# Performance work log

Measured on AMD Instinct MI355X. Metric: run time of the kernel, lower is better.

The kernel has to match this reference:

```python
import jax, jax.numpy as jnp
import numpy as np

B, T, D, H = 4, 2048, 1024, 16
HD = D // H  # head_dim = 64


def setup_inputs() -> dict:
    key = jax.random.key(0)
    ks = jax.random.split(key, 5)
    s = 0.02
    return {
        "x": jax.random.normal(ks[0], (B, T, D), dtype=jnp.float32),
        "Wq": jax.random.normal(ks[1], (D, D), dtype=jnp.float32) * s,
        "Wk": jax.random.normal(ks[2], (D, D), dtype=jnp.float32) * s,
        "Wv": jax.random.normal(ks[3], (D, D), dtype=jnp.float32) * s,
        "Wp": jax.random.normal(ks[4], (D, D), dtype=jnp.float32) * s,
    }


def reference(x, Wq, Wk, Wv, Wp):
    b, t, d = x.shape
    # QKV projections (bias=False), reshape to (b, h, t, hd)
    q = (x @ Wq.T).reshape(b, t, H, HD).transpose(0, 2, 1, 3)
    k = (x @ Wk.T).reshape(b, t, H, HD).transpose(0, 2, 1, 3)
    v = (x @ Wv.T).reshape(b, t, H, HD).transpose(0, 2, 1, 3)
    # scaled scores with causal mask
    scores = jnp.einsum("bhqd,bhkd->bhqk", q, k) / jnp.sqrt(jnp.float32(HD))
    causal = jnp.triu(jnp.ones((t, t), dtype=bool), k=1)
    scores = jnp.where(causal, -jnp.inf, scores)
    weights = jax.nn.softmax(scores, axis=-1)
    # dropout = 0.0 / eval mode -> identity
    ctx = jnp.einsum("bhqk,bhkd->bhqd", weights, v)
    ctx = ctx.transpose(0, 2, 1, 3).reshape(b, t, d)
    return ctx @ Wp.T
```

## Files before the change

### kernel.cpp

```cpp
#include <hip/hip_runtime.h>

typedef unsigned short u16;
typedef unsigned int u32;
typedef __attribute__((ext_vector_type(8))) short short8;
typedef __attribute__((ext_vector_type(4))) short short4_t;
typedef __attribute__((ext_vector_type(4))) float float4_t;

#define T_SEQ 2048
#define DMODEL 1024
#define NH 16
#define HD 64

#define GLL16(g, l) __builtin_amdgcn_global_load_lds( \
    (const __attribute__((address_space(1))) u32*)(g), \
    (__attribute__((address_space(3))) u32*)(l), 16, 0, 0)

__device__ inline u16 f2b(float f) {
  u32 x = __builtin_bit_cast(u32, f);
  x += 0x7fffu + ((x >> 16) & 1u);
  return (u16)(x >> 16);
}

__global__ __launch_bounds__(256) void conv_f2b(
    const float* __restrict__ x, const float* __restrict__ wq,
    const float* __restrict__ wk, const float* __restrict__ wv,
    const float* __restrict__ wp, u16* __restrict__ xb, u16* __restrict__ wb) {
  const size_t SZc = (size_t)8192 * 1024, WSZc = (size_t)1024 * 1024;
  size_t i = ((size_t)blockIdx.x * 256 + threadIdx.x) * 8;
  const float* s; u16* d; size_t off;
  if (i < SZc) { s = x; d = xb; off = i; }
  else {
    size_t j = i - SZc;
    size_t w = j >> 20;
    off = j & (WSZc - 1);
    s = (w == 0) ? wq : (w == 1) ? wk : (w == 2) ? wv : wp;
    d = wb + w * WSZc;
  }
  float4_t a = *(const float4_t*)(s + off);
  float4_t b = *(const float4_t*)(s + off + 4);
  short8 o;
  o[0] = (short)f2b(a[0]); o[1] = (short)f2b(a[1]);
  o[2] = (short)f2b(a[2]); o[3] = (short)f2b(a[3]);
  o[4] = (short)f2b(b[0]); o[5] = (short)f2b(b[1]);
  o[6] = (short)f2b(b[2]); o[7] = (short)f2b(b[3]);
  *(short8*)(d + off) = o;
}

__global__ __launch_bounds__(256) void gemm_bt(
    const u16* __restrict__ A,
    const u16* __restrict__ B0, const u16* __restrict__ B1, const u16* __restrict__ B2,
    u16* __restrict__ C0, u16* __restrict__ C1, u16* __restrict__ C2,
    float* __restrict__ Cf,
    int N, int Kd, int vtz, int of32, int scz, float cscale)
{
  const u16* Bp = (blockIdx.z == 0) ? B0 : ((blockIdx.z == 1) ? B1 : B2);
  u16* Cp = (blockIdx.z == 0) ? C0 : ((blockIdx.z == 1) ? C1 : C2);
  const bool vt = ((int)blockIdx.z == vtz);
  const float cs = ((int)blockIdx.z == scz) ? cscale : 1.0f;
  __shared__ u16 As[128 * 32];
  __shared__ u16 Bs[128 * 32];
  const int tid = threadIdx.x;
  const int lane = tid & 63;
  const int li = lane & 15;
  const int quad = lane >> 4;
  const int wv = tid >> 6;
  const int wm = (wv >> 1) * 64;
  const int wn = (wv & 1) * 64;
  const size_t bm = (size_t)blockIdx.x * 128;
  const size_t bn = (size_t)blockIdx.y * 128;

  float4_t acc[4][4];
  const float4_t z4 = {0.f, 0.f, 0.f, 0.f};
#pragma unroll
  for (int i = 0; i < 4; i++)
#pragma unroll
    for (int j = 0; j < 4; j++) acc[i][j] = z4;

  const int c0 = tid, c1 = tid + 256;
  const int r0 = c0 >> 2, e0 = (c0 & 3) * 8;
  const int r1 = c1 >> 2, e1 = (c1 & 3) * 8;

  for (int k0 = 0; k0 < Kd; k0 += 32) {
    __syncthreads();
    GLL16(A + (bm + r0) * Kd + k0 + e0, &As[c0 * 8]);
    GLL16(A + (bm + r1) * Kd + k0 + e1, &As[c1 * 8]);
    GLL16(Bp + (bn + r0) * Kd + k0 + e0, &Bs[c0 * 8]);
    GLL16(Bp + (bn + r1) * Kd + k0 + e1, &Bs[c1 * 8]);
    __syncthreads();
    short8 af[4], bf[4];
#pragma unroll
    for (int i = 0; i < 4; i++)
      af[i] = *(const short8*)&As[(wm + i * 16 + li) * 32 + quad * 8];
#pragma unroll
    for (int j = 0; j < 4; j++)
      bf[j] = *(const short8*)&Bs[(wn + j * 16 + li) * 32 + quad * 8];
#pragma unroll
    for (int i = 0; i < 4; i++)
#pragma unroll
      for (int j = 0; j < 4; j++)
        acc[i][j] = __builtin_amdgcn_mfma_f32_16x16x32_bf16(bf[j], af[i], acc[i][j], 0, 0, 0);
  }

  if (of32) {
#pragma unroll
    for (int i = 0; i < 4; i++)
#pragma unroll
      for (int j = 0; j < 4; j++) {
        size_t row = bm + wm + (size_t)(i * 16 + li);
        size_t col = bn + wn + (size_t)(j * 16 + quad * 4);
        *(float4_t*)&Cf[row * (size_t)N + col] = acc[i][j];
      }
  } else if (!vt) {
#pragma unroll
    for (int i = 0; i < 4; i++)
#pragma unroll
      for (int j = 0; j < 4; j++) {
        size_t row = bm + wm + (size_t)(i * 16 + li);
        size_t col = bn + wn + (size_t)(j * 16 + quad * 4);
        short4_t o;
#pragma unroll
        for (int r = 0; r < 4; r++) o[r] = (short)f2b(acc[i][j][r] * cs);
        *(short4_t*)&Cp[row * (size_t)N + col] = o;
      }
  } else {
#pragma unroll
    for (int i = 0; i < 4; i++) {
      size_t row = bm + wm + (size_t)(i * 16 + li);
      size_t bb = row >> 11;
      size_t tt = row & 2047;
#pragma unroll
      for (int j = 0; j < 4; j++) {
        size_t col = bn + wn + (size_t)(j * 16 + quad * 4);
#pragma unroll
        for (int r = 0; r < 4; r++)
          Cp[(bb * 1024 + col + r) * 2048 + tt] = f2b(acc[i][j][r]);
      }
    }
  }
}

#define LROW 72
__global__ __launch_bounds__(512) void attn_fwd(const u16* __restrict__ Qb,
                                                const u16* __restrict__ Kb,
                                                const u16* __restrict__ Vtb,
                                                u16* __restrict__ Ob) {
  __shared__ u16 Qs[128 * LROW];
  __shared__ u16 Kds[2][64 * LROW];
  __shared__ u16 Vds[2][64 * LROW];
  const int bh = blockIdx.y;
  const int bidx = bh >> 4;
  const int tid = threadIdx.x;
  const int lane = tid & 63;
  const int wv = tid >> 6;
  const int li = lane & 15;
  const int quad = lane >> 4;
  const size_t qkBase = ((size_t)bidx * T_SEQ) * DMODEL + (size_t)(bh & 15) * HD;
  const size_t vBase = (size_t)bh * HD * T_SEQ;
  const int krow = tid >> 3;
  const int kc8 = (tid & 7) * 8;
  const int kld = krow * LROW + kc8;
  const float4_t z4 = {0.f, 0.f, 0.f, 0.f};

#pragma unroll 1
  for (int ph = 0; ph < 2; ph++) {
    const int qblk = ph ? (int)blockIdx.x : (15 - (int)blockIdx.x);
    const int q0 = qblk * 128;
    const int ktmax = 2 * qblk + 1;
    const int qg0 = q0 + wv * 16;

    __syncthreads();
#pragma unroll
    for (int t = 0; t < 4; t++) {
      int slot = tid + t * 512;
      int row = slot >> 4, hc = slot & 15;
      *(short4_t*)&Qs[row * LROW + hc * 4] =
          *(const short4_t*)&Qb[qkBase + (size_t)(q0 + row) * DMODEL + hc * 4];
    }
    short8 kpre = *(const short8*)&Kb[qkBase + (size_t)krow * DMODEL + kc8];
    short8 vpre = *(const short8*)&Vtb[vBase + (size_t)krow * T_SEQ + kc8];
    __syncthreads();
    short8 qf[2];
    {
      const int row = wv * 16 + li;
#pragma unroll
      for (int s = 0; s < 2; s++)
        qf[s] = *(const short8*)&Qs[row * LROW + s * 32 + quad * 8];
    }
    *(short8*)&Kds[0][kld] = kpre;
    *(short8*)&Vds[0][kld] = vpre;
    kpre = *(const short8*)&Kb[qkBase + (size_t)(64 + krow) * DMODEL + kc8];
    vpre = *(const short8*)&Vtb[vBase + (size_t)krow * T_SEQ + 64 + kc8];

    float4_t accO[4];
#pragma unroll
    for (int dt = 0; dt < 4; dt++) accO[dt] = z4;
    float l_i = 0.f;

    for (int kt = 0; kt <= ktmax; kt++) {
      const int k0 = kt * 64;
      const int cb = kt & 1;
      __syncthreads();
      if (kt < ktmax) {
        *(short8*)&Kds[cb ^ 1][kld] = kpre;
        *(short8*)&Vds[cb ^ 1][kld] = vpre;
        if (kt + 1 < ktmax) {
          const int kn = k0 + 128;
          kpre = *(const short8*)&Kb[qkBase + (size_t)(kn + krow) * DMODEL + kc8];
          vpre = *(const short8*)&Vtb[vBase + (size_t)krow * T_SEQ + kn + kc8];
        }
      }
      if (k0 > qg0 + 15) continue;

      float4_t st[4];
#pragma unroll
      for (int jt = 0; jt < 4; jt++) {
        float4_t c4 = z4;
        const int row = jt * 16 + li;
#pragma unroll
        for (int s = 0; s < 2; s++) {
          short8 kf = *(const short8*)&Kds[cb][row * LROW + s * 32 + quad * 8];
          c4 = __builtin_amdgcn_mfma_f32_16x16x32_bf16(kf, qf[s], c4, 0, 0, 0);
        }
        st[jt] = c4;
      }

      short4_t pf[4];
      if (k0 + 63 > qg0) {
        const int ig = qg0 + li;
#pragma unroll
        for (int jt = 0; jt < 4; jt++)
#pragma unroll
          for (int r = 0; r < 4; r++) {
            int jg = k0 + jt * 16 + quad * 4 + r;
            float p = (jg <= ig) ? __builtin_amdgcn_exp2f(st[jt][r]) : 0.f;
            l_i += p;
            pf[jt][r] = (short)(__builtin_bit_cast(u32, p) >> 16);
          }
      } else {
#pragma unroll
        for (int jt = 0; jt < 4; jt++)
#pragma unroll
          for (int r = 0; r < 4; r++) {
            float p = __builtin_amdgcn_exp2f(st[jt][r]);
            l_i += p;
            pf[jt][r] = (short)(__builtin_bit_cast(u32, p) >> 16);
          }
      }

#pragma unroll
      for (int dt = 0; dt < 4; dt++) {
        const int d = dt * 16 + li;
#pragma unroll
        for (int jt = 0; jt < 4; jt++) {
          short4_t vf = *(const short4_t*)&Vds[cb][d * LROW + jt * 16 + quad * 4];
          accO[dt] = __builtin_amdgcn_mfma_f32_16x16x16bf16_1k(vf, pf[jt], accO[dt], 0, 0, 0);
        }
      }
    }

    l_i += __shfl_xor(l_i, 16);
    l_i += __shfl_xor(l_i, 32);
    const float inv = 1.f / l_i;
    const int orow = q0 + wv * 16 + li;
    const size_t obase = ((size_t)bidx * T_SEQ + orow) * DMODEL + (size_t)(bh & 15) * HD;
#pragma unroll
    for (int dt = 0; dt < 4; dt++) {
      short4_t o4;
#pragma unroll
      for (int r = 0; r < 4; r++) o4[r] = (short)f2b(accO[dt][r] * inv);
      *(short4_t*)&Ob[obase + dt * 16 + quad * 4] = o4;
    }
  }
}

extern "C" void kernel_launch(void* const* d_in, const int* in_sizes, int n_in,
                              void* d_out, int out_size, void* d_ws, size_t ws_size,
                              hipStream_t stream) {
  (void)in_sizes; (void)n_in; (void)out_size; (void)ws_size;
  const float* x  = (const float*)d_in[0];
  const float* Wq = (const float*)d_in[1];
  const float* Wk = (const float*)d_in[2];
  const float* Wv = (const float*)d_in[3];
  const float* Wp = (const float*)d_in[4];
  float* out = (float*)d_out;

  const size_t SZ  = (size_t)8192 * 1024;
  const size_t WSZ = (size_t)1024 * 1024;

  u16* xb  = (u16*)d_ws;
  u16* wb  = xb + SZ;
  u16* Q   = wb + 4 * WSZ;
  u16* Kp  = Q + SZ;
  u16* Vt  = Kp + SZ;
  u16* ctx = Vt + SZ;

  const float SC = 0.18033688011112042f;

  dim3 blk(256);
  conv_f2b<<<dim3((unsigned)((SZ + 4 * WSZ) / 8 / 256)), blk, 0, stream>>>(
      x, Wq, Wk, Wv, Wp, xb, wb);
  gemm_bt<<<dim3(64, 8, 3), blk, 0, stream>>>(
      xb, wb, wb + WSZ, wb + 2 * WSZ, Q, Kp, Vt, nullptr, DMODEL, DMODEL, 2, 0,
      0, SC);
  attn_fwd<<<dim3(8, 4 * NH), dim3(512), 0, stream>>>(Q, Kp, Vt, ctx);
  gemm_bt<<<dim3(64, 8, 1), blk, 0, stream>>>(
      ctx, wb + 3 * WSZ, nullptr, nullptr, nullptr, nullptr, nullptr, out,
      DMODEL, DMODEL, -1, 1, -1, 1.0f);
}
```

Measured before the change: 250.4 us.

## Add dedicated 256x256-tile QKV GEMM kernel with 512 threads and swizzled LDS

Replaces the generic gemm_bt launch for the Q/K/V projections with a new gemm_qkv kernel. It uses 256x256 output tiles and 8 waves, each computing a 128x64 sub-tile, with XOR-swizzled double-buffered LDS staging through global_load_lds. Inner-loop MFMA blocks are wrapped in s_setprio, and Q/K outputs are written as vectorized short4 stores. The larger tiles raise operand reuse and cut global loads, in exchange for higher register pressure (128 accumulator floats per thread) and only 384 blocks.

```diff
diff --git a/kernel.cpp b/kernel.cpp
--- a/kernel.cpp
+++ b/kernel.cpp
@@ -139,6 +139,184 @@
   }
 }
 
+__global__ __launch_bounds__(512, 2) void gemm_qkv(
+    const u16* __restrict__ A,
+    const u16* __restrict__ B0, const u16* __restrict__ B1,
+    const u16* __restrict__ B2,
+    u16* __restrict__ C0, u16* __restrict__ C1, u16* __restrict__ C2,
+    float sc) {
+  __shared__ u16 Ls[2][2][2][8192];
+  const int z = blockIdx.z;
+  const u16* __restrict__ Bp = (z == 0) ? B0 : (z == 1) ? B1 : B2;
+  u16* __restrict__ Cp = (z == 0) ? C0 : (z == 1) ? C1 : C2;
+  const float cs = (z == 0) ? sc : 1.0f;
+  const int tid = threadIdx.x;
+  const int lane = tid & 63;
+  const int li = lane & 15;
+  const int quad = lane >> 4;
+  const int wid = tid >> 6;
+  const int wm = wid >> 2;
+  const int wnq = wid & 3;
+  const int wnh = wnq >> 1;
+  const int wbo = (wnq & 1) * 64;
+  const size_t bm = (size_t)blockIdx.x * 256;
+  const size_t bn = (size_t)blockIdx.y * 256;
+
+  const int xs0 = (quad ^ (li & 7)) * 16;
+  const int xs1 = ((4 + quad) ^ (li & 7)) * 16;
+
+  const int sr0 = tid >> 3;
+  const int sg0 = ((tid & 7) ^ (sr0 & 7)) * 8;
+  const int sr1 = (tid + 512) >> 3;
+  const int sg1 = (((tid + 512) & 7) ^ (sr1 & 7)) * 8;
+
+  auto stage = [&](int db, int k0) {
+    const size_t ka = (size_t)k0;
+    GLL16(A  + (bm + sr0) * 1024 + ka + sg0,       &Ls[db][0][0][tid * 8]);
+    GLL16(A  + (bm + 128 + sr0) * 1024 + ka + sg0, &Ls[db][0][1][tid * 8]);
+    GLL16(Bp + (bn + sr0) * 1024 + ka + sg0,       &Ls[db][1][0][tid * 8]);
+    GLL16(Bp + (bn + 128 + sr0) * 1024 + ka + sg0, &Ls[db][1][1][tid * 8]);
+    GLL16(A  + (bm + sr1) * 1024 + ka + sg1,       &Ls[db][0][0][(tid + 512) * 8]);
+    GLL16(A  + (bm + 128 + sr1) * 1024 + ka + sg1, &Ls[db][0][1][(tid + 512) * 8]);
+    GLL16(Bp + (bn + sr1) * 1024 + ka + sg1,       &Ls[db][1][0][(tid + 512) * 8]);
+    GLL16(Bp + (bn + 128 + sr1) * 1024 + ka + sg1, &Ls[db][1][1][(tid + 512) * 8]);
+  };
+
+  float4_t acc[8][4];
+  const float4_t z4 = {0.f, 0.f, 0.f, 0.f};
+#pragma unroll
+  for (int i = 0; i < 8; ++i)
+#pragma unroll
+    for (int j = 0; j < 4; ++j) acc[i][j] = z4;
+
+  stage(0, 0);
+
+#pragma unroll 1
+  for (int t = 0; t < 16; ++t) {
+    const int b = t & 1;
+    if (t < 15) {
+      stage(b ^ 1, (t + 1) * 64);
+      asm volatile("s_waitcnt vmcnt(8)" ::: "memory");
+    } else {
+      asm volatile("s_waitcnt vmcnt(0)" ::: "memory");
+    }
+    __builtin_amdgcn_s_barrier();
+    asm volatile("" ::: "memory");
+
+    const char* Ab = (const char*)&Ls[b][0][wm][0];
+    const char* Bb = (const char*)&Ls[b][1][wnh][0];
+    short8 af[2][4], bf[2][2];
+
+#pragma unroll
+    for (int kk = 0; kk < 2; ++kk) {
+      const int xs = kk ? xs1 : xs0;
+#pragma unroll
+      for (int i = 0; i < 4; ++i)
+        af[kk][i] = *(const short8*)(Ab + (i * 16 + li) * 128 + xs);
+#pragma unroll
+      for (int j = 0; j < 2; ++j)
+        bf[kk][j] = *(const short8*)(Bb + (wbo + j * 16 + li) * 128 + xs);
+    }
+    __builtin_amdgcn_s_setprio(1);
+#pragma unroll
+    for (int i = 0; i < 4; ++i)
+#pragma unroll
+      for (int j = 0; j < 2; ++j)
+#pragma unroll
+        for (int kk = 0; kk < 2; ++kk)
+          acc[i][j] = __builtin_amdgcn_mfma_f32_16x16x32_bf16(
+              bf[kk][j], af[kk][i], acc[i][j], 0, 0, 0);
+    __builtin_amdgcn_s_setprio(0);
+
+#pragma unroll
+    for (int kk = 0; kk < 2; ++kk) {
+      const int xs = kk ? xs1 : xs0;
+#pragma unroll
+      for (int j = 0; j < 2; ++j)
+        bf[kk][j] = *(const short8*)(Bb + (wbo + (2 + j) * 16 + li) * 128 + xs);
+    }
+    __builtin_amdgcn_s_setprio(1);
+#pragma unroll
+    for (int i = 0; i < 4; ++i)
+#pragma unroll
+      for (int j = 0; j < 2; ++j)
+#pragma unroll
+        for (int kk = 0; kk < 2; ++kk)
+          acc[i][2 + j] = __builtin_amdgcn_mfma_f32_16x16x32_bf16(
+              bf[kk][j], af[kk][i], acc[i][2 + j], 0, 0, 0);
+    __builtin_amdgcn_s_setprio(0);
+
+#pragma unroll
+    for (int kk = 0; kk < 2; ++kk) {
+      const int xs = kk ? xs1 : xs0;
+#pragma unroll
+      for (int i = 0; i < 4; ++i)
+        af[kk][i] = *(const short8*)(Ab + ((4 + i) * 16 + li) * 128 + xs);
+    }
+    __builtin_amdgcn_s_setprio(1);
+#pragma unroll
+    for (int i = 0; i < 4; ++i)
+#pragma unroll
+      for (int j = 0; j < 2; ++j)
+#pragma unroll
+        for (int kk = 0; kk < 2; ++kk)
+          acc[4 + i][2 + j] = __builtin_amdgcn_mfma_f32_16x16x32_bf16(
+              bf[kk][j], af[kk][i], acc[4 + i][2 + j], 0, 0, 0);
+    __builtin_amdgcn_s_setprio(0);
+
+#pragma unroll
+    for (int kk = 0; kk < 2; ++kk) {
+      const int xs = kk ? xs1 : xs0;
+#pragma unroll
+      for (int j = 0; j < 2; ++j)
+        bf[kk][j] = *(const short8*)(Bb + (wbo + j * 16 + li) * 128 + xs);
+    }
+    __builtin_amdgcn_s_setprio(1);
+#pragma unroll
+    for (int i = 0; i < 4; ++i)
+#pragma unroll
+      for (int j = 0; j < 2; ++j)
+#pragma unroll
+        for (int kk = 0; kk < 2; ++kk)
+          acc[4 + i][j] = __builtin_amdgcn_mfma_f32_16x16x32_bf16(
+              bf[kk][j], af[kk][i], acc[4 + i][j], 0, 0, 0);
+    __builtin_amdgcn_s_setprio(0);
+
+    asm volatile("" ::: "memory");
+    __builtin_amdgcn_s_barrier();
+  }
+
+  const size_t cb = bn + (size_t)wnq * 64;
+  if (z != 2) {
+#pragma unroll
+    for (int i = 0; i < 8; ++i) {
+      const size_t row = bm + (size_t)(wm * 128 + i * 16 + li);
+#pragma unroll
+      for (int j = 0; j < 4; ++j) {
+        const size_t col = cb + (size_t)(j * 16 + quad * 4);
+        short4_t o;
+#pragma unroll
+        for (int r = 0; r < 4; ++r) o[r] = (short)f2b(acc[i][j][r] * cs);
+        *(short4_t*)&Cp[row * 1024 + col] = o;
+      }
+    }
+  } else {
+#pragma unroll
+    for (int i = 0; i < 8; ++i) {
+      const size_t row = bm + (size_t)(wm * 128 + i * 16 + li);
+      const size_t bb = row >> 11;
+      const size_t tt = row & 2047;
+#pragma unroll
+      for (int j = 0; j < 4; ++j) {
+        const size_t col = cb + (size_t)(j * 16 + quad * 4);
+#pragma unroll
+        for (int r = 0; r < 4; ++r)
+          Cp[(bb * 1024 + col + r) * 2048 + tt] = f2b(acc[i][j][r]);
+      }
+    }
+  }
+}
+
 #define LROW 72
 __global__ __launch_bounds__(512) void attn_fwd(const u16* __restrict__ Qb,
                                                 const u16* __restrict__ Kb,
@@ -299,9 +477,8 @@
   dim3 blk(256);
   conv_f2b<<<dim3((unsigned)((SZ + 4 * WSZ) / 8 / 256)), blk, 0, stream>>>(
       x, Wq, Wk, Wv, Wp, xb, wb);
-  gemm_bt<<<dim3(64, 8, 3), blk, 0, stream>>>(
-      xb, wb, wb + WSZ, wb + 2 * WSZ, Q, Kp, Vt, nullptr, DMODEL, DMODEL, 2, 0,
-      0, SC);
+  gemm_qkv<<<dim3(32, 4, 3), dim3(512), 0, stream>>>(
+      xb, wb, wb + WSZ, wb + 2 * WSZ, Q, Kp, Vt, SC);
   attn_fwd<<<dim3(8, 4 * NH), dim3(512), 0, stream>>>(Q, Kp, Vt, ctx);
   gemm_bt<<<dim3(64, 8, 1), blk, 0, stream>>>(
       ctx, wb + 3 * WSZ, nullptr, nullptr, nullptr, nullptr, nullptr, out,
```

New measurement: 251.2 us. No clear change (+0.3%).

## Add dedicated 256x256-tile QKV GEMM with triple-buffered direct-to-LDS loads

Applied to the files above, without the earlier changes.

Replaces the generic gemm_bt launch for the QKV projections with a new gemm_qkv kernel using 512 threads, 256x256 output tiles, an XOR-swizzled LDS layout and a three-stage global_load_lds pipeline that interleaves staging with MFMA work under s_setprio. Larger tiles raise arithmetic intensity and cut global traffic per FLOP. The grid drops to 384 blocks, which may underfill the GPU's compute units, and the large LDS and accumulator footprint may limit occupancy. The V output still uses scattered transposed 2-byte stores.

```diff
diff --git a/kernel.cpp b/kernel.cpp
--- a/kernel.cpp
+++ b/kernel.cpp
@@ -139,6 +139,135 @@
   }
 }
 
+__global__ __launch_bounds__(512, 2) void gemm_qkv(
+    const u16* __restrict__ A,
+    const u16* __restrict__ B0, const u16* __restrict__ B1,
+    const u16* __restrict__ B2,
+    u16* __restrict__ C0, u16* __restrict__ C1, u16* __restrict__ C2,
+    float sc) {
+  __shared__ u16 Ls[3][2][2][4096];
+  const int z = blockIdx.z;
+  const u16* __restrict__ Bp = (z == 0) ? B0 : (z == 1) ? B1 : B2;
+  u16* __restrict__ Cp = (z == 0) ? C0 : (z == 1) ? C1 : C2;
+  const float cs = (z == 0) ? sc : 1.0f;
+  const int tid = threadIdx.x;
+  const int lane = tid & 63;
+  const int li = lane & 15;
+  const int quad = lane >> 4;
+  const int wid = tid >> 6;
+  const int wm = wid >> 2;
+  const int wnq = wid & 3;
+  const int wnh = wnq >> 1;
+  const int wbo = (wnq & 1) * 64;
+  const size_t bm = (size_t)blockIdx.x * 256;
+  const size_t bn = (size_t)blockIdx.y * 256;
+
+  const int xsA = (quad ^ ((li >> 1) & 3)) * 16;
+
+  const int srow = tid >> 2;
+  const int sgx = (((tid & 3) ^ ((tid >> 3) & 3)) * 8);
+
+  float4_t acc[8][4];
+  const float4_t z4 = {0.f, 0.f, 0.f, 0.f};
+#pragma unroll
+  for (int i = 0; i < 8; ++i)
+#pragma unroll
+    for (int j = 0; j < 4; ++j) acc[i][j] = z4;
+
+  auto stageA = [&](int s, int t, int h) {
+    GLL16(A + (bm + (size_t)(h * 128 + srow)) * 1024 + (size_t)(t * 32) + sgx,
+          &Ls[s][0][h][tid * 8]);
+  };
+  auto stageB = [&](int s, int t, int h) {
+    GLL16(Bp + (bn + (size_t)(h * 128 + srow)) * 1024 + (size_t)(t * 32) + sgx,
+          &Ls[s][1][h][tid * 8]);
+  };
+
+  stageA(0, 0, 0); stageA(0, 0, 1); stageB(0, 0, 0); stageB(0, 0, 1);
+  stageA(1, 1, 0); stageA(1, 1, 1); stageB(1, 1, 0); stageB(1, 1, 1);
+  asm volatile("s_waitcnt vmcnt(4)" ::: "memory");
+  __builtin_amdgcn_s_barrier();
+
+  int cbuf = 0, sbuf = 2;
+#pragma unroll 1
+  for (int t = 0; t < 32; ++t) {
+    const bool doStage = (t < 30);
+    const char* Ab = (const char*)&Ls[cbuf][0][wm][0];
+    const char* Bb = (const char*)&Ls[cbuf][1][wnh][0];
+    short8 af[4], bf[4];
+
+#pragma unroll
+    for (int i = 0; i < 4; ++i)
+      af[i] = *(const short8*)(Ab + (i * 16 + li) * 64 + xsA);
+#pragma unroll
+    for (int j = 0; j < 4; ++j)
+      bf[j] = *(const short8*)(Bb + (wbo + j * 16 + li) * 64 + xsA);
+    if (doStage) { stageA(sbuf, t + 2, 0); stageA(sbuf, t + 2, 1); }
+    __builtin_amdgcn_s_barrier();
+    asm volatile("s_waitcnt lgkmcnt(0)" ::: "memory");
+    __builtin_amdgcn_s_setprio(1);
+#pragma unroll
+    for (int i = 0; i < 4; ++i)
+#pragma unroll
+      for (int j = 0; j < 4; ++j)
+        acc[i][j] = __builtin_amdgcn_mfma_f32_16x16x32_bf16(
+            bf[j], af[i], acc[i][j], 0, 0, 0);
+    __builtin_amdgcn_s_setprio(0);
+    __builtin_amdgcn_s_barrier();
+
+#pragma unroll
+    for (int i = 0; i < 4; ++i)
+      af[i] = *(const short8*)(Ab + ((4 + i) * 16 + li) * 64 + xsA);
+    if (doStage) { stageB(sbuf, t + 2, 0); stageB(sbuf, t + 2, 1); }
+    __builtin_amdgcn_s_barrier();
+    asm volatile("s_waitcnt lgkmcnt(0)" ::: "memory");
+    __builtin_amdgcn_s_setprio(1);
+#pragma unroll
+    for (int i = 0; i < 4; ++i)
+#pragma unroll
+      for (int j = 0; j < 4; ++j)
+        acc[4 + i][j] = __builtin_amdgcn_mfma_f32_16x16x32_bf16(
+            bf[j], af[i], acc[4 + i][j], 0, 0, 0);
+    __builtin_amdgcn_s_setprio(0);
+    if (doStage) asm volatile("s_waitcnt vmcnt(4)" ::: "memory");
+    else         asm volatile("s_waitcnt vmcnt(0)" ::: "memory");
+    __builtin_amdgcn_s_barrier();
+
+    cbuf = (cbuf == 2) ? 0 : cbuf + 1;
+    sbuf = (sbuf == 2) ? 0 : sbuf + 1;
+  }
+
+  const size_t colb = bn + (size_t)wnq * 64;
+  if (z != 2) {
+#pragma unroll
+    for (int i = 0; i < 8; ++i) {
+      const size_t row = bm + (size_t)(wm * 128 + i * 16 + li);
+#pragma unroll
+      for (int j = 0; j < 4; ++j) {
+        const size_t col = colb + (size_t)(j * 16 + quad * 4);
+        short4_t o;
+#pragma unroll
+        for (int r = 0; r < 4; ++r) o[r] = (short)f2b(acc[i][j][r] * cs);
+        *(short4_t*)&Cp[row * 1024 + col] = o;
+      }
+    }
+  } else {
+#pragma unroll
+    for (int i = 0; i < 8; ++i) {
+      const size_t row = bm + (size_t)(wm * 128 + i * 16 + li);
+      const size_t bb = row >> 11;
+      const size_t tt = row & 2047;
+#pragma unroll
+      for (int j = 0; j < 4; ++j) {
+        const size_t col = colb + (size_t)(j * 16 + quad * 4);
+#pragma unroll
+        for (int r = 0; r < 4; ++r)
+          Cp[(bb * 1024 + col + r) * 2048 + tt] = f2b(acc[i][j][r]);
+      }
+    }
+  }
+}
+
 #define LROW 72
 __global__ __launch_bounds__(512) void attn_fwd(const u16* __restrict__ Qb,
                                                 const u16* __restrict__ Kb,
@@ -299,9 +428,8 @@
   dim3 blk(256);
   conv_f2b<<<dim3((unsigned)((SZ + 4 * WSZ) / 8 / 256)), blk, 0, stream>>>(
       x, Wq, Wk, Wv, Wp, xb, wb);
-  gemm_bt<<<dim3(64, 8, 3), blk, 0, stream>>>(
-      xb, wb, wb + WSZ, wb + 2 * WSZ, Q, Kp, Vt, nullptr, DMODEL, DMODEL, 2, 0,
-      0, SC);
+  gemm_qkv<<<dim3(32, 4, 3), dim3(512), 0, stream>>>(
+      xb, wb, wb + WSZ, wb + 2 * WSZ, Q, Kp, Vt, SC);
   attn_fwd<<<dim3(8, 4 * NH), dim3(512), 0, stream>>>(Q, Kp, Vt, ctx);
   gemm_bt<<<dim3(64, 8, 1), blk, 0, stream>>>(
       ctx, wb + 3 * WSZ, nullptr, nullptr, nullptr, nullptr, nullptr, out,
```

Result: no change. 252.8 us (+1.0%).

## Add 256x256-tile ping-pong pipelined QKV GEMM with explicit barriers

Applied to the files above, without the earlier changes.

Replaces the generic gemm_bt launch for the QKV projections with a dedicated 512-thread kernel that uses 256x256 output tiles. Operands are staged with double-buffered, XOR-swizzled direct global-to-LDS loads, and the work is split into half-tile phases. Manual s_waitcnt, barriers and setprio let MFMA work overlap with loads for the next k-tile. This aims at better data reuse and latency hiding in the largest GEMM, at the cost of heavy LDS use (128KB) and fragile hand-tuned synchronisation that limits occupancy to one or two blocks per CU. The grid also shrinks to 384 blocks, which may leave some CUs unevenly loaded.

```diff
diff --git a/kernel.cpp b/kernel.cpp
--- a/kernel.cpp
+++ b/kernel.cpp
@@ -14,6 +14,13 @@
 #define GLL16(g, l) __builtin_amdgcn_global_load_lds( \
     (const __attribute__((address_space(1))) u32*)(g), \
     (__attribute__((address_space(3))) u32*)(l), 16, 0, 0)
+
+#define PH_BAR() do { asm volatile("" ::: "memory"); \
+    __builtin_amdgcn_s_barrier(); \
+    asm volatile("" ::: "memory"); } while (0)
+#define WAIT_LGKM0() asm volatile("s_waitcnt lgkmcnt(0)" ::: "memory")
+#define WAIT_VM4() asm volatile("s_waitcnt vmcnt(4)" ::: "memory")
+#define WAIT_VM0() asm volatile("s_waitcnt vmcnt(0)" ::: "memory")
 
 __device__ inline u16 f2b(float f) {
   u32 x = __builtin_bit_cast(u32, f);
@@ -139,6 +146,168 @@
   }
 }
 
+__global__ __launch_bounds__(512, 2) void gemm_qkv(
+    const u16* __restrict__ Ap,
+    const u16* __restrict__ B0w, const u16* __restrict__ B1w,
+    const u16* __restrict__ B2w,
+    u16* __restrict__ C0, u16* __restrict__ C1, u16* __restrict__ C2,
+    float sc) {
+  __shared__ u16 Als[2][2][8192];
+  __shared__ u16 Bls[2][2][8192];
+  const int z = blockIdx.z;
+  const u16* __restrict__ Bp = (z == 0) ? B0w : (z == 1) ? B1w : B2w;
+  u16* __restrict__ Cp = (z == 0) ? C0 : (z == 1) ? C1 : C2;
+  const float cs = (z == 0) ? sc : 1.0f;
+  const int tid = threadIdx.x;
+  const int lane = tid & 63;
+  const int li = lane & 15;
+  const int quad = lane >> 4;
+  const int wid = tid >> 6;
+  const int wr = wid >> 2;
+  const int wc = wid & 3;
+  const size_t bm = (size_t)blockIdx.x * 256;
+  const size_t bn = (size_t)blockIdx.y * 256;
+
+  const int xs0 = (quad ^ (li & 7)) * 16;
+  const int lrA = wr * 64 + li;
+  const int lrB = wc * 32 + li;
+
+  const int srow = tid >> 3;
+  const int cswz8 = ((tid & 7) ^ (srow & 7)) * 8;
+
+  auto stageA = [&](int db, int h, int tk) {
+#pragma unroll
+    for (int u = 0; u < 2; ++u) {
+      int lr = u * 64 + srow;
+      size_t grow = bm + (size_t)((lr >> 6) * 128 + h * 64 + (lr & 63));
+      GLL16(Ap + grow * 1024 + (size_t)(tk * 64) + cswz8,
+            &Als[db][h][u * 4096 + tid * 8]);
+    }
+  };
+  auto stageB = [&](int db, int p, int tk) {
+#pragma unroll
+    for (int u = 0; u < 2; ++u) {
+      int lr = u * 64 + srow;
+      size_t grow = bn + (size_t)((lr >> 5) * 64 + p * 32 + (lr & 31));
+      GLL16(Bp + grow * 1024 + (size_t)(tk * 64) + cswz8,
+            &Bls[db][p][u * 4096 + tid * 8]);
+    }
+  };
+
+  float4_t acc[8][4];
+  const float4_t z4 = {0.f, 0.f, 0.f, 0.f};
+#pragma unroll
+  for (int i = 0; i < 8; ++i)
+#pragma unroll
+    for (int j = 0; j < 4; ++j) acc[i][j] = z4;
+
+  short8 af[2][4], bf0[2][2], bf1[2][2];
+
+#define LDA(DB, H) \
+  { const char* base = (const char*)&Als[DB][H][0]; \
+    _Pragma("unroll") for (int ii = 0; ii < 4; ++ii) { \
+      af[0][ii] = *(const short8*)(base + (size_t)(lrA + ii * 16) * 128 + xs0); \
+      af[1][ii] = *(const short8*)(base + (size_t)(lrA + ii * 16) * 128 + (xs0 ^ 64)); } }
+#define LDB(DB, P, BF) \
+  { const char* base = (const char*)&Bls[DB][P][0]; \
+    _Pragma("unroll") for (int jj = 0; jj < 2; ++jj) { \
+      BF[0][jj] = *(const short8*)(base + (size_t)(lrB + jj * 16) * 128 + xs0); \
+      BF[1][jj] = *(const short8*)(base + (size_t)(lrB + jj * 16) * 128 + (xs0 ^ 64)); } }
+#define MFMA16(I0, J0, BF) \
+  __builtin_amdgcn_s_setprio(1); \
+  _Pragma("unroll") for (int ii = 0; ii < 4; ++ii) \
+  _Pragma("unroll") for (int jj = 0; jj < 2; ++jj) \
+  _Pragma("unroll") for (int ks = 0; ks < 2; ++ks) \
+    acc[I0 + ii][J0 + jj] = __builtin_amdgcn_mfma_f32_16x16x32_bf16( \
+        BF[ks][jj], af[ks][ii], acc[I0 + ii][J0 + jj], 0, 0, 0); \
+  __builtin_amdgcn_s_setprio(0)
+
+  stageA(0, 0, 0); stageB(0, 0, 0); stageA(0, 1, 0); stageB(0, 1, 0);
+  stageA(1, 0, 1); stageB(1, 1, 1);
+  WAIT_VM4();
+  PH_BAR();
+
+  const int NT = 16;
+#pragma unroll 1
+  for (int it = 0; it < 8; ++it) {
+    const int t1 = 2 * it + 1, t2 = 2 * it + 2, t3 = 2 * it + 3;
+    const bool s2 = (t2 < NT), s3 = (t3 < NT);
+
+    LDA(0, 0); LDB(0, 0, bf0);
+    stageA(1, 1, t1);
+    PH_BAR(); WAIT_LGKM0();
+    MFMA16(0, 0, bf0);
+    PH_BAR();
+    LDB(0, 1, bf1);
+    stageB(1, 0, t1);
+    PH_BAR(); WAIT_LGKM0();
+    MFMA16(0, 2, bf1);
+    PH_BAR();
+    LDA(0, 1);
+    if (s2) stageA(0, 0, t2);
+    PH_BAR(); WAIT_LGKM0();
+    MFMA16(4, 2, bf1);
+    PH_BAR();
+    if (s2) { stageB(0, 1, t2); WAIT_VM4(); } else { WAIT_VM0(); }
+    PH_BAR();
+    MFMA16(4, 0, bf0);
+    PH_BAR();
+
+    LDA(1, 0); LDB(1, 0, bf0);
+    if (s2) stageA(0, 1, t2);
+    PH_BAR(); WAIT_LGKM0();
+    MFMA16(0, 0, bf0);
+    PH_BAR();
+    LDB(1, 1, bf1);
+    if (s2) stageB(0, 0, t2);
+    PH_BAR(); WAIT_LGKM0();
+    MFMA16(0, 2, bf1);
+    PH_BAR();
+    LDA(1, 1);
+    if (s3) stageA(1, 0, t3);
+    PH_BAR(); WAIT_LGKM0();
+    MFMA16(4, 2, bf1);
+    PH_BAR();
+    if (s3) { stageB(1, 1, t3); WAIT_VM4(); } else { WAIT_VM0(); }
+    PH_BAR();
+    MFMA16(4, 0, bf0);
+    PH_BAR();
+  }
+#undef LDA
+#undef LDB
+#undef MFMA16
+
+  const size_t colb = bn + (size_t)wc * 64;
+  if (z != 2) {
+#pragma unroll
+    for (int i = 0; i < 8; ++i) {
+      const size_t row = bm + (size_t)(wr * 128 + i * 16 + li);
+#pragma unroll
+      for (int j = 0; j < 4; ++j) {
+        const size_t col = colb + (size_t)(j * 16 + quad * 4);
+        short4_t o;
+#pragma unroll
+        for (int r = 0; r < 4; ++r) o[r] = (short)f2b(acc[i][j][r] * cs);
+        *(short4_t*)&Cp[row * 1024 + col] = o;
+      }
+    }
+  } else {
+#pragma unroll
+    for (int i = 0; i < 8; ++i) {
+      const size_t row = bm + (size_t)(wr * 128 + i * 16 + li);
+      const size_t bb = row >> 11;
+      const size_t tt = row & 2047;
+#pragma unroll
+      for (int j = 0; j < 4; ++j) {
+        const size_t col = colb + (size_t)(j * 16 + quad * 4);
+#pragma unroll
+        for (int r = 0; r < 4; ++r)
+          Cp[(bb * 1024 + col + r) * 2048 + tt] = f2b(acc[i][j][r]);
+      }
+    }
+  }
+}
+
 #define LROW 72
 __global__ __launch_bounds__(512) void attn_fwd(const u16* __restrict__ Qb,
                                                 const u16* __restrict__ Kb,
@@ -299,9 +468,8 @@
   dim3 blk(256);
   conv_f2b<<<dim3((unsigned)((SZ + 4 * WSZ) / 8 / 256)), blk, 0, stream>>>(
       x, Wq, Wk, Wv, Wp, xb, wb);
-  gemm_bt<<<dim3(64, 8, 3), blk, 0, stream>>>(
-      xb, wb, wb + WSZ, wb + 2 * WSZ, Q, Kp, Vt, nullptr, DMODEL, DMODEL, 2, 0,
-      0, SC);
+  gemm_qkv<<<dim3(32, 4, 3), dim3(512), 0, stream>>>(
+      xb, wb, wb + WSZ, wb + 2 * WSZ, Q, Kp, Vt, SC);
   attn_fwd<<<dim3(8, 4 * NH), dim3(512), 0, stream>>>(Q, Kp, Vt, ctx);
   gemm_bt<<<dim3(64, 8, 1), blk, 0, stream>>>(
       ctx, wb + 3 * WSZ, nullptr, nullptr, nullptr, nullptr, nullptr, out,
```

Result: no change. 251.1 us (+0.3%).
